# Kernel tuning notes

Hardware: AMD Instinct MI355X
Metric: run time of the kernel (lower is better)

## Reference

```python
import jax, jax.numpy as jnp
import numpy as np

B, S, F, U = 64, 512, 128, 512          # seq_length == units (required for broadcast in original code)
SIGDIM = F + F * F                       # level-2 truncated signature dimension
GRID_SIZE, SPLINE_ORDER = 5, 3           # efficient-KAN style defaults
NB = GRID_SIZE + SPLINE_ORDER            # number of b-spline basis functions per input feature
LN_EPS = 1e-3                            # keras LayerNormalization default epsilon


def _make_grid():
    h = 2.0 / GRID_SIZE  # uniform grid on [-1, 1], extended by spline order
    return -1.0 + h * jnp.arange(-SPLINE_ORDER, GRID_SIZE + SPLINE_ORDER + 1, dtype=jnp.float32)


def _b_splines(x, grid):
    # x: (N, F) -> (N, F, NB) via Cox-de Boor recursion
    x = x[..., None]
    bases = ((x >= grid[:-1]) & (x < grid[1:])).astype(x.dtype)
    for p in range(1, SPLINE_ORDER + 1):
        left = (x - grid[:-(p + 1)]) / (grid[p:-1] - grid[:-(p + 1)])
        right = (grid[p + 1:] - x) / (grid[p + 1:] - grid[1:-p])
        bases = left * bases[..., :-1] + right * bases[..., 1:]
    return bases


def _kan_linear(x, base_w, spline_w, grid):
    # KANLinear, no bias / no layernorm: silu base branch + b-spline branch
    lead = x.shape[:-1]
    base = jax.nn.silu(x) @ base_w                                  # (..., U)
    b = _b_splines(x.reshape(-1, x.shape[-1]), grid)                # (N, F, NB)
    spl = jnp.einsum('nfk,ufk->nu', b, spline_w).reshape(*lead, base_w.shape[1])
    return base + spl


def _signature2(x):
    # level-2 path signature of piecewise-linear path x: (B, S, F) -> (B, F + F*F)
    dx = x[:, 1:] - x[:, :-1]                                       # (B, S-1, F)
    s1 = dx.sum(axis=1)                                             # (B, F)
    cs = jnp.cumsum(dx, axis=1)
    prev = jnp.concatenate([jnp.zeros_like(cs[:, :1]), cs[:, :-1]], axis=1)
    s2 = jnp.einsum('bti,btj->bij', prev + 0.5 * dx, dx)            # (B, F, F)
    return jnp.concatenate([s1, s2.reshape(x.shape[0], -1)], axis=-1)


def _grkan(sig, w1, b1, w2, b2, w3, b3, w4, b4, ws, bs, gamma, beta):
    # gated residual network mapping signature -> softmax attention weights (B, U)
    h = jax.nn.elu(sig @ w1 + b1)
    h = h @ w2 + b2
    glu = jax.nn.sigmoid(h @ w3 + b3) * (h @ w4 + b4)
    y = sig @ ws + bs + glu
    mu = jnp.mean(y, axis=-1, keepdims=True)
    var = jnp.var(y, axis=-1, keepdims=True)
    y = (y - mu) / jnp.sqrt(var + LN_EPS) * gamma + beta
    return jax.nn.softmax(y, axis=-1)


def setup_inputs() -> dict:
    key = jax.random.key(0)
    ks = jax.random.split(key, 24)
    n = lambda k, shp, s=0.02: jax.random.normal(k, shp, dtype=jnp.float32) * s
    inp = {
        'inputs': jax.random.normal(ks[0], (B, S, F), dtype=jnp.float32),
        'h_prev': jax.random.normal(ks[1], (B, U), dtype=jnp.float32),
        'c_prev': jax.random.normal(ks[2], (B, U), dtype=jnp.float32),
        'time_kernel': n(ks[3], (S, 1), 0.1),
        'kan_base_w': n(ks[4], (F, U)),
        'kan_spline_w': n(ks[5], (U, F, NB)),
        'g_w1': n(ks[6], (SIGDIM, U)), 'g_b1': jnp.zeros((U,), jnp.float32),
        'g_w2': n(ks[7], (U, U)), 'g_b2': jnp.zeros((U,), jnp.float32),
        'g_w3': n(ks[8], (U, U)), 'g_b3': jnp.zeros((U,), jnp.float32),
        'g_w4': n(ks[9], (U, U)), 'g_b4': jnp.zeros((U,), jnp.float32),
        'g_skip_w': n(ks[10], (SIGDIM, U)), 'g_skip_b': jnp.zeros((U,), jnp.float32),
        'ln_gamma': jnp.ones((U,), jnp.float32), 'ln_beta': jnp.zeros((U,), jnp.float32),
        'wf': n(ks[11], (2 * U, U)), 'bf': jnp.zeros((U,), jnp.float32),
        'wi': n(ks[12], (2 * U, U)), 'bi': jnp.zeros((U,), jnp.float32),
        'wc': n(ks[13], (2 * U, U)), 'bc': jnp.zeros((U,), jnp.float32),
        'wo': n(ks[14], (2 * U, U)), 'bo': jnp.zeros((U,), jnp.float32),
    }
    return inp


def reference(inputs, h_prev, c_prev, time_kernel, kan_base_w, kan_spline_w,
              g_w1, g_b1, g_w2, g_b2, g_w3, g_b3, g_w4, g_b4, g_skip_w, g_skip_b,
              ln_gamma, ln_beta, wf, bf, wi, bi, wc, bc, wo, bo):
    grid = _make_grid()
    weighted = time_kernel * inputs                                  # (B,S,F)
    sig = _signature2(weighted)                                      # (B,SIGDIM)
    attn = _grkan(sig, g_w1, g_b1, g_w2, g_b2, g_w3, g_b3, g_w4, g_b4,
                  g_skip_w, g_skip_b, ln_gamma, ln_beta)             # (B,S) since U==S
    kan_out = _kan_linear(weighted, kan_base_w, kan_spline_w, grid)  # (B,S,U)
    attended = kan_out * attn[..., None]                             # (B,S,U)
    current = attended.mean(axis=1)                                  # (B,U)
    combined = jnp.concatenate([current, h_prev], axis=-1)           # (B,2U)
    f = jax.nn.sigmoid(combined @ wf + bf)
    i = jax.nn.sigmoid(combined @ wi + bi)
    cand = jnp.tanh(combined @ wc + bc)
    o = jax.nn.sigmoid(combined @ wo + bo)
    c_new = f * c_prev + i * cand
    h_new = o * jnp.tanh(c_new)
    return h_new, c_new
```

## Files before the change

kernel.cpp:

```cpp
#include <hip/hip_runtime.h>
#include <math.h>

#define BB 64
#define SS 512
#define FF 128
#define UU 512
#define NBB 8
#define SIGDIM (FF + FF*FF)
#define K3 16512
#define KK 1152
#define NCH 32

typedef __attribute__((ext_vector_type(8))) __bf16 bf16x8;
typedef __attribute__((ext_vector_type(4))) float f32x4;

__device__ __forceinline__ unsigned short f2bf(float x) {
    unsigned int u = __float_as_uint(x);
    unsigned int r = u + 0x7FFFu + ((u >> 16) & 1u);
    return (unsigned short)(r >> 16);
}

__device__ __forceinline__ float sigmoidf(float x) { return 1.0f / (1.0f + expf(-x)); }

__global__ void k_wprep(const float* __restrict__ splw, const float* __restrict__ basew,
                        const float* __restrict__ h_prev,
                        unsigned short* __restrict__ Wt, unsigned short* __restrict__ comb_b) {
    int idx = blockIdx.x * 256 + threadIdx.x;
    if (idx >= UU * KK) return;
    int u = idx / KK, c = idx % KK;
    float v = (c < 1024) ? splw[(size_t)u * 1024 + c] : basew[(size_t)(c - 1024) * UU + u];
    Wt[idx] = f2bf(v);
    if (idx < BB * UU) {
        int b = idx >> 9, uu = idx & 511;
        comb_b[(size_t)b * 1024 + 512 + uu] = f2bf(h_prev[idx]);
    }
}

__global__ __launch_bounds__(256) void k_wt3(const float* __restrict__ w2, const float* __restrict__ w3,
                                             const float* __restrict__ w4, const float* __restrict__ wf,
                                             const float* __restrict__ wi, const float* __restrict__ wc,
                                             const float* __restrict__ wo,
                                             unsigned short* __restrict__ W2t,
                                             unsigned short* __restrict__ W3t,
                                             unsigned short* __restrict__ W4t,
                                             unsigned short* __restrict__ Wgt) {
    int kt = blockIdx.x, ut = blockIdx.y, z = blockIdx.z;
    int Kdim = (z < 3) ? 512 : 1024;
    if (kt * 64 >= Kdim) return;
    const float* src;
    unsigned short* dst;
    switch (z) {
        case 0: src = w2; dst = W2t; break;
        case 1: src = w3; dst = W3t; break;
        case 2: src = w4; dst = W4t; break;
        case 3: src = wf; dst = Wgt; break;
        case 4: src = wi; dst = Wgt + (size_t)512 * 1024; break;
        case 5: src = wc; dst = Wgt + (size_t)1024 * 1024; break;
        default: src = wo; dst = Wgt + (size_t)1536 * 1024; break;
    }
    __shared__ float tile[64][65];
    int tid = threadIdx.x;
    int k0 = kt * 64, u0 = ut * 64;
#pragma unroll
    for (int p = 0; p < 16; ++p) {
        int e = p * 256 + tid;
        int kk = e >> 6, uu = e & 63;
        tile[kk][uu] = src[(size_t)(k0 + kk) * UU + u0 + uu];
    }
    __syncthreads();
#pragma unroll
    for (int p = 0; p < 16; ++p) {
        int e = p * 256 + tid;
        int uu = e >> 6, kk = e & 63;
        dst[(size_t)(u0 + uu) * Kdim + k0 + kk] = f2bf(tile[kk][uu]);
    }
}

__global__ __launch_bounds__(256) void k_wt2(const float* __restrict__ w1,
                                             const float* __restrict__ gsw,
                                             unsigned short* __restrict__ W1t,
                                             unsigned short* __restrict__ Wst) {
    int kt = blockIdx.x, ut = blockIdx.y, mat = blockIdx.z;
    const float* src = mat ? gsw : w1;
    unsigned short* dst = mat ? Wst : W1t;
    __shared__ float tile[64][65];
    int tid = threadIdx.x;
    int k0 = kt * 64, u0 = ut * 64;
#pragma unroll
    for (int p = 0; p < 16; ++p) {
        int e = p * 256 + tid;
        int kk = e >> 6, uu = e & 63;
        tile[kk][uu] = src[(size_t)(k0 + kk) * UU + u0 + uu];
    }
    __syncthreads();
#pragma unroll
    for (int p = 0; p < 16; ++p) {
        int e = p * 256 + tid;
        int uu = e >> 6, kk = e & 63;
        dst[(size_t)(u0 + uu) * K3 + k0 + kk] = f2bf(tile[kk][uu]);
    }
}

__global__ __launch_bounds__(256) void k_adprep(const float* __restrict__ inp,
                                                const float* __restrict__ tk,
                                                unsigned short* __restrict__ aT,
                                                unsigned short* __restrict__ dT) {
    int tt0 = blockIdx.x * 64, f0 = blockIdx.y * 64, b = blockIdx.z;
    __shared__ float aS[64][65], dS[64][65];
    __shared__ float tkS[65];
    int tid = threadIdx.x;
    if (tid < 65) { int t = tt0 + tid; tkS[tid] = (t < SS) ? tk[t] : 0.f; }
    __syncthreads();
    const float* ib = inp + (size_t)b * SS * FF;
    float tk0 = tk[0];
    for (int e = tid; e < 64 * 64; e += 256) {
        int tt = e >> 6, ff = e & 63;
        int t = tt0 + tt;
        int f = f0 + ff;
        float av = 0.f, dv = 0.f;
        if (t < SS - 1) {
            float wa = tkS[tt] * ib[(size_t)t * FF + f];
            float wn = tkS[tt + 1] * ib[(size_t)(t + 1) * FF + f];
            float w0 = tk0 * ib[f];
            av = 0.5f * (wa + wn) - w0;
            dv = wn - wa;
        }
        aS[tt][ff] = av; dS[tt][ff] = dv;
    }
    __syncthreads();
    for (int e = tid; e < 64 * 64; e += 256) {
        int ff = e >> 6, tt = e & 63;
        size_t o = ((size_t)b * FF + f0 + ff) * SS + tt0 + tt;
        aT[o] = f2bf(aS[tt][ff]);
        dT[o] = f2bf(dS[tt][ff]);
    }
}

__global__ __launch_bounds__(256) void k_sig_mfma(const unsigned short* __restrict__ aT,
                                                  const unsigned short* __restrict__ dT,
                                                  float* __restrict__ s2part) {
    int kc = blockIdx.x, b = blockIdx.y;
    int tid = threadIdx.x, lane = tid & 63;
    int wv = __builtin_amdgcn_readfirstlane(tid >> 6);
    int wrow = (wv & 1) * 64, wcol = (wv >> 1) * 64;
    int k0 = kc * 128;
    const unsigned short* pa = aT + ((size_t)b * FF + wrow + (lane & 15)) * SS + k0 + (lane >> 4) * 8;
    const unsigned short* pd = dT + ((size_t)b * FF + wcol + (lane & 15)) * SS + k0 + (lane >> 4) * 8;
    f32x4 acc[4][4];
#pragma unroll
    for (int i = 0; i < 4; ++i)
#pragma unroll
        for (int j = 0; j < 4; ++j) acc[i][j] = (f32x4)(0.f);
#pragma unroll
    for (int t = 0; t < 4; ++t) {
        bf16x8 af[4], df[4];
#pragma unroll
        for (int rt = 0; rt < 4; ++rt) af[rt] = *(const bf16x8*)(pa + (size_t)rt * 16 * SS + t * 32);
#pragma unroll
        for (int ct = 0; ct < 4; ++ct) df[ct] = *(const bf16x8*)(pd + (size_t)ct * 16 * SS + t * 32);
#pragma unroll
        for (int rt = 0; rt < 4; ++rt)
#pragma unroll
            for (int ct = 0; ct < 4; ++ct)
                acc[rt][ct] = __builtin_amdgcn_mfma_f32_16x16x32_bf16(af[rt], df[ct], acc[rt][ct], 0, 0, 0);
    }
    float* outp = s2part + ((size_t)kc * BB + b) * (FF * FF);
    int quad = lane >> 4, col = lane & 15;
#pragma unroll
    for (int rt = 0; rt < 4; ++rt)
#pragma unroll
        for (int ct = 0; ct < 4; ++ct)
#pragma unroll
            for (int reg = 0; reg < 4; ++reg)
                outp[(wrow + rt * 16 + quad * 4 + reg) * FF + wcol + ct * 16 + col] = acc[rt][ct][reg];
}

__global__ void k_sig_reduce(const float* __restrict__ inp, const float* __restrict__ tk,
                             const float* __restrict__ s2part, unsigned short* __restrict__ sigb) {
    int idx = blockIdx.x * 256 + threadIdx.x;
    if (idx >= BB * SIGDIM) return;
    int b = idx / SIGDIM, r = idx % SIGDIM;
    float v;
    if (r < FF) {
        v = tk[SS - 1] * inp[((size_t)b * SS + SS - 1) * FF + r] - tk[0] * inp[(size_t)b * SS * FF + r];
    } else {
        int ij = r - FF;
        v = 0.f;
#pragma unroll
        for (int c = 0; c < 4; ++c) v += s2part[((size_t)c * BB + b) * (FF * FF) + ij];
    }
    sigb[idx] = f2bf(v);
}

__global__ __launch_bounds__(64) void k_sig_direct(const unsigned short* __restrict__ sigb,
                                                   const unsigned short* __restrict__ W1t,
                                                   const unsigned short* __restrict__ Wst,
                                                   const float* __restrict__ b1,
                                                   unsigned short* __restrict__ h1b,
                                                   float* __restrict__ skippre) {
    int lane = threadIdx.x;
    int mt = blockIdx.x, nt = blockIdx.y, mat = blockIdx.z;
    const unsigned short* Bp = mat ? Wst : W1t;
    const unsigned short* pa = sigb + (size_t)(mt * 16 + (lane & 15)) * K3 + (lane >> 4) * 8;
    const unsigned short* pb = Bp + (size_t)(nt * 16 + (lane & 15)) * K3 + (lane >> 4) * 8;
    f32x4 acc0 = (f32x4)(0.f), acc1 = (f32x4)(0.f);
#pragma unroll 8
    for (int t = 0; t < K3 / 32; t += 2) {
        bf16x8 a0 = *(const bf16x8*)(pa + t * 32);
        bf16x8 b0 = *(const bf16x8*)(pb + t * 32);
        bf16x8 a1 = *(const bf16x8*)(pa + t * 32 + 32);
        bf16x8 b1v = *(const bf16x8*)(pb + t * 32 + 32);
        acc0 = __builtin_amdgcn_mfma_f32_16x16x32_bf16(a0, b0, acc0, 0, 0, 0);
        acc1 = __builtin_amdgcn_mfma_f32_16x16x32_bf16(a1, b1v, acc1, 0, 0, 0);
    }
    int col = lane & 15, quad = lane >> 4;
    int j = nt * 16 + col;
    if (mat == 0) {
        float bb = b1[j];
#pragma unroll
        for (int reg = 0; reg < 4; ++reg) {
            int row = mt * 16 + quad * 4 + reg;
            float v = acc0[reg] + acc1[reg] + bb;
            h1b[(size_t)row * UU + j] = f2bf(v > 0.f ? v : expf(v) - 1.0f);
        }
    } else {
#pragma unroll
        for (int reg = 0; reg < 4; ++reg) {
            int row = mt * 16 + quad * 4 + reg;
            skippre[(size_t)row * UU + j] = acc0[reg] + acc1[reg];
        }
    }
}

__global__ __launch_bounds__(64) void k_h2_direct(const unsigned short* __restrict__ h1b,
                                                  const unsigned short* __restrict__ W2t,
                                                  const float* __restrict__ b2,
                                                  unsigned short* __restrict__ h2b) {
    int lane = threadIdx.x;
    int mt = blockIdx.x, nt = blockIdx.y;
    const unsigned short* pa = h1b + (size_t)(mt * 16 + (lane & 15)) * 512 + (lane >> 4) * 8;
    const unsigned short* pb = W2t + (size_t)(nt * 16 + (lane & 15)) * 512 + (lane >> 4) * 8;
    f32x4 acc0 = (f32x4)(0.f), acc1 = (f32x4)(0.f);
#pragma unroll
    for (int t = 0; t < 16; t += 2) {
        bf16x8 a0 = *(const bf16x8*)(pa + t * 32);
        bf16x8 b0 = *(const bf16x8*)(pb + t * 32);
        bf16x8 a1 = *(const bf16x8*)(pa + t * 32 + 32);
        bf16x8 b1v = *(const bf16x8*)(pb + t * 32 + 32);
        acc0 = __builtin_amdgcn_mfma_f32_16x16x32_bf16(a0, b0, acc0, 0, 0, 0);
        acc1 = __builtin_amdgcn_mfma_f32_16x16x32_bf16(a1, b1v, acc1, 0, 0, 0);
    }
    int col = lane & 15, quad = lane >> 4;
    int j = nt * 16 + col;
    float bb = b2[j];
#pragma unroll
    for (int reg = 0; reg < 4; ++reg) {
        int row = mt * 16 + quad * 4 + reg;
        h2b[(size_t)row * UU + j] = f2bf(acc0[reg] + acc1[reg] + bb);
    }
}

__global__ __launch_bounds__(64) void k_glu_direct(const unsigned short* __restrict__ h2b,
                                                   const unsigned short* __restrict__ W3t,
                                                   const unsigned short* __restrict__ W4t,
                                                   const float* __restrict__ b3,
                                                   const float* __restrict__ b4,
                                                   const float* __restrict__ skippre,
                                                   const float* __restrict__ skb,
                                                   float* __restrict__ yv) {
    int lane = threadIdx.x;
    int mt = blockIdx.x, nt = blockIdx.y;
    const unsigned short* pa = h2b + (size_t)(mt * 16 + (lane & 15)) * 512 + (lane >> 4) * 8;
    const unsigned short* pb3 = W3t + (size_t)(nt * 16 + (lane & 15)) * 512 + (lane >> 4) * 8;
    const unsigned short* pb4 = W4t + (size_t)(nt * 16 + (lane & 15)) * 512 + (lane >> 4) * 8;
    f32x4 acc3 = (f32x4)(0.f), acc4 = (f32x4)(0.f);
#pragma unroll
    for (int t = 0; t < 16; ++t) {
        bf16x8 a = *(const bf16x8*)(pa + t * 32);
        bf16x8 b3f = *(const bf16x8*)(pb3 + t * 32);
        bf16x8 b4f = *(const bf16x8*)(pb4 + t * 32);
        acc3 = __builtin_amdgcn_mfma_f32_16x16x32_bf16(a, b3f, acc3, 0, 0, 0);
        acc4 = __builtin_amdgcn_mfma_f32_16x16x32_bf16(a, b4f, acc4, 0, 0, 0);
    }
    int col = lane & 15, quad = lane >> 4;
    int j = nt * 16 + col;
    float bb3 = b3[j], bb4 = b4[j], sb = skb[j];
#pragma unroll
    for (int reg = 0; reg < 4; ++reg) {
        int row = mt * 16 + quad * 4 + reg;
        float g = sigmoidf(acc3[reg] + bb3);
        yv[(size_t)row * UU + j] = skippre[(size_t)row * UU + j] + sb + g * (acc4[reg] + bb4);
    }
}

__device__ __forceinline__ float block_sum(float v, float* red) {
    int tid = threadIdx.x;
#pragma unroll
    for (int off = 32; off > 0; off >>= 1) v += __shfl_down(v, off);
    __syncthreads();
    if ((tid & 63) == 0) red[tid >> 6] = v;
    __syncthreads();
    float r = red[0];
#pragma unroll
    for (int i = 1; i < 8; ++i) r += red[i];
    return r;
}
__device__ __forceinline__ float block_max(float v, float* red) {
    int tid = threadIdx.x;
#pragma unroll
    for (int off = 32; off > 0; off >>= 1) v = fmaxf(v, __shfl_down(v, off));
    __syncthreads();
    if ((tid & 63) == 0) red[tid >> 6] = v;
    __syncthreads();
    float r = red[0];
#pragma unroll
    for (int i = 1; i < 8; ++i) r = fmaxf(r, red[i]);
    return r;
}

__global__ void k_lnsm(const float* __restrict__ yv, const float* __restrict__ gamma,
                       const float* __restrict__ beta, float* __restrict__ attn) {
    int b = blockIdx.x, u = threadIdx.x;
    __shared__ float red[8];
    float v = yv[(size_t)b * UU + u];
    float mu = block_sum(v, red) * (1.0f / UU);
    float d = v - mu;
    float var = block_sum(d * d, red) * (1.0f / UU);
    float z = d * rsqrtf(var + 1e-3f) * gamma[u] + beta[u];
    float m = block_max(z, red);
    float e = expf(z - m);
    float Z = block_sum(e, red);
    attn[(size_t)b * UU + u] = e / Z;
}

__global__ __launch_bounds__(128) void k_attn_red(const float* __restrict__ inp,
                                                  const float* __restrict__ tk,
                                                  const float* __restrict__ attn,
                                                  float* __restrict__ Apart) {
    int b = blockIdx.x, ch = blockIdx.y;
    int f = threadIdx.x;
    __shared__ float attnS[16], tkS[16];
    if (f < 16) { attnS[f] = attn[(size_t)b * UU + ch * 16 + f]; tkS[f] = tk[ch * 16 + f]; }
    __syncthreads();
    const float* ib = inp + ((size_t)b * SS + ch * 16) * FF + f;
    float acc[9] = {};
#pragma unroll
    for (int s = 0; s < 16; ++s) {
        float w = tkS[s] * ib[(size_t)s * FF];
        float a = attnS[s];
        float t = (w + 2.2f) * 2.5f;
        float cf = floorf(fminf(fmaxf(t, -2.f), 13.f));
        int c = (int)cf;
        float u = t - cf;
        float u2 = u * u, u3 = u2 * u;
        float p0 = u3 * (1.f / 6.f);
        float p1 = (-3.f * u3 + 3.f * u2 + 3.f * u + 1.f) * (1.f / 6.f);
        float p2 = (3.f * u3 - 6.f * u2 + 4.f) * (1.f / 6.f);
        float onemu = 1.f - u;
        float p3 = onemu * onemu * onemu * (1.f / 6.f);
#pragma unroll
        for (int k2 = 0; k2 < 8; ++k2) {
            int d = c - k2;
            float v = (d == 0) ? p0 : (d == 1) ? p1 : (d == 2) ? p2 : (d == 3) ? p3 : 0.f;
            acc[k2] += a * v;
        }
        acc[8] += a * (w * sigmoidf(w));
    }
    float* op = Apart + ((size_t)ch * BB + b) * KK;
    float4 v0 = { acc[0], acc[1], acc[2], acc[3] };
    float4 v1 = { acc[4], acc[5], acc[6], acc[7] };
    *(float4*)(op + f * 8) = v0;
    *(float4*)(op + f * 8 + 4) = v1;
    op[1024 + f] = acc[8];
}

__global__ void k_ared_red(const float* __restrict__ Apart, unsigned short* __restrict__ Aredb) {
    int idx = blockIdx.x * 256 + threadIdx.x;
    if (idx >= BB * KK) return;
    int b = idx / KK, c = idx % KK;
    float s = 0.f;
#pragma unroll
    for (int ch = 0; ch < NCH; ++ch) s += Apart[((size_t)ch * BB + b) * KK + c];
    Aredb[idx] = f2bf(s * (1.0f / SS));
}

__global__ __launch_bounds__(64) void k_cur_direct(const unsigned short* __restrict__ Aredb,
                                                   const unsigned short* __restrict__ Wt,
                                                   unsigned short* __restrict__ comb_b) {
    int lane = threadIdx.x;
    int mt = blockIdx.x, nt = blockIdx.y;
    const unsigned short* pa = Aredb + (size_t)(mt * 16 + (lane & 15)) * KK + (lane >> 4) * 8;
    const unsigned short* pb = Wt + (size_t)(nt * 16 + (lane & 15)) * KK + (lane >> 4) * 8;
    f32x4 acc0 = (f32x4)(0.f), acc1 = (f32x4)(0.f);
#pragma unroll 6
    for (int t = 0; t < KK / 32; t += 2) {
        bf16x8 a0 = *(const bf16x8*)(pa + t * 32);
        bf16x8 b0 = *(const bf16x8*)(pb + t * 32);
        bf16x8 a1 = *(const bf16x8*)(pa + t * 32 + 32);
        bf16x8 b1v = *(const bf16x8*)(pb + t * 32 + 32);
        acc0 = __builtin_amdgcn_mfma_f32_16x16x32_bf16(a0, b0, acc0, 0, 0, 0);
        acc1 = __builtin_amdgcn_mfma_f32_16x16x32_bf16(a1, b1v, acc1, 0, 0, 0);
    }
    int col = lane & 15, quad = lane >> 4;
    int j = nt * 16 + col;
#pragma unroll
    for (int reg = 0; reg < 4; ++reg) {
        int row = mt * 16 + quad * 4 + reg;
        comb_b[(size_t)row * 1024 + j] = f2bf(acc0[reg] + acc1[reg]);
    }
}

__global__ __launch_bounds__(64) void k_gates_direct(const unsigned short* __restrict__ comb_b,
                                                     const unsigned short* __restrict__ Wgt,
                                                     float* __restrict__ gates) {
    int lane = threadIdx.x;
    int mt = blockIdx.x, nt = blockIdx.y;
    const unsigned short* pa = comb_b + (size_t)(mt * 16 + (lane & 15)) * 1024 + (lane >> 4) * 8;
    const unsigned short* pb = Wgt + (size_t)(nt * 16 + (lane & 15)) * 1024 + (lane >> 4) * 8;
    f32x4 acc0 = (f32x4)(0.f), acc1 = (f32x4)(0.f);
#pragma unroll 8
    for (int t = 0; t < 32; t += 2) {
        bf16x8 a0 = *(const bf16x8*)(pa + t * 32);
        bf16x8 b0 = *(const bf16x8*)(pb + t * 32);
        bf16x8 a1 = *(const bf16x8*)(pa + t * 32 + 32);
        bf16x8 b1v = *(const bf16x8*)(pb + t * 32 + 32);
        acc0 = __builtin_amdgcn_mfma_f32_16x16x32_bf16(a0, b0, acc0, 0, 0, 0);
        acc1 = __builtin_amdgcn_mfma_f32_16x16x32_bf16(a1, b1v, acc1, 0, 0, 0);
    }
    int col = lane & 15, quad = lane >> 4;
    int j = nt * 16 + col;
#pragma unroll
    for (int reg = 0; reg < 4; ++reg) {
        int row = mt * 16 + quad * 4 + reg;
        gates[(size_t)row * 2048 + j] = acc0[reg] + acc1[reg];
    }
}

__global__ void k_cell(const float* __restrict__ gates,
                       const float* __restrict__ bf_, const float* __restrict__ bi_,
                       const float* __restrict__ bc_, const float* __restrict__ bo_,
                       const float* __restrict__ c_prev, float* __restrict__ out) {
    int idx = blockIdx.x * 256 + threadIdx.x;
    if (idx >= BB * UU) return;
    int b = idx >> 9, u = idx & 511;
    const float* g = gates + (size_t)b * 2048;
    float f = sigmoidf(g[u] + bf_[u]);
    float ii = sigmoidf(g[512 + u] + bi_[u]);
    float cd = tanhf(g[1024 + u] + bc_[u]);
    float o = sigmoidf(g[1536 + u] + bo_[u]);
    float cn = f * c_prev[idx] + ii * cd;
    out[idx] = o * tanhf(cn);
    out[(size_t)BB * UU + idx] = cn;
}

extern "C" void kernel_launch(void* const* d_in, const int* in_sizes, int n_in,
                              void* d_out, int out_size, void* d_ws, size_t ws_size,
                              hipStream_t stream) {
    const float* inp   = (const float*)d_in[0];
    const float* hprev = (const float*)d_in[1];
    const float* cprev = (const float*)d_in[2];
    const float* tk    = (const float*)d_in[3];
    const float* basew = (const float*)d_in[4];
    const float* splw  = (const float*)d_in[5];
    const float* gw1   = (const float*)d_in[6];
    const float* gb1   = (const float*)d_in[7];
    const float* gw2   = (const float*)d_in[8];
    const float* gb2   = (const float*)d_in[9];
    const float* gw3   = (const float*)d_in[10];
    const float* gb3   = (const float*)d_in[11];
    const float* gw4   = (const float*)d_in[12];
    const float* gb4   = (const float*)d_in[13];
    const float* gsw   = (const float*)d_in[14];
    const float* gsb   = (const float*)d_in[15];
    const float* lng   = (const float*)d_in[16];
    const float* lnb   = (const float*)d_in[17];
    const float* wf    = (const float*)d_in[18];
    const float* bf_   = (const float*)d_in[19];
    const float* wi    = (const float*)d_in[20];
    const float* bi_   = (const float*)d_in[21];
    const float* wc    = (const float*)d_in[22];
    const float* bc_   = (const float*)d_in[23];
    const float* wo    = (const float*)d_in[24];
    const float* bo_   = (const float*)d_in[25];
    float* out = (float*)d_out;

    float* ws = (float*)d_ws;
    size_t o = 0;
    unsigned short* W1t = (unsigned short*)(ws + o); o += (size_t)UU * K3 / 2;
    unsigned short* Wst = (unsigned short*)(ws + o); o += (size_t)UU * K3 / 2;
    unsigned short* Wt  = (unsigned short*)(ws + o); o += (size_t)UU * KK / 2;
    float* s2part   = ws + o; o += (size_t)4 * BB * FF * FF;
    unsigned short* aT = (unsigned short*)(ws + o); o += (size_t)BB * FF * SS / 2;
    unsigned short* dT = (unsigned short*)(ws + o); o += (size_t)BB * FF * SS / 2;
    unsigned short* sigb = (unsigned short*)(ws + o); o += (size_t)BB * K3 / 2;
    float* skippre  = ws + o; o += (size_t)BB * UU;
    unsigned short* h1b = (unsigned short*)(ws + o); o += (size_t)BB * UU / 2;
    unsigned short* h2b = (unsigned short*)(ws + o); o += (size_t)BB * UU / 2;
    float* yv       = ws + o; o += (size_t)BB * UU;
    float* attn     = ws + o; o += (size_t)BB * UU;
    float* Apart    = ws + o; o += (size_t)NCH * BB * KK;
    unsigned short* Aredb = (unsigned short*)(ws + o); o += (size_t)BB * KK / 2;
    unsigned short* W2t = (unsigned short*)(ws + o); o += (size_t)512 * 512 / 2;
    unsigned short* W3t = (unsigned short*)(ws + o); o += (size_t)512 * 512 / 2;
    unsigned short* W4t = (unsigned short*)(ws + o); o += (size_t)512 * 512 / 2;
    unsigned short* Wgt = (unsigned short*)(ws + o); o += (size_t)2048 * 1024 / 2;
    unsigned short* comb_b = (unsigned short*)(ws + o); o += (size_t)BB * 1024 / 2;
    float* gates    = ws + o; o += (size_t)BB * 2048;
    (void)ws_size; (void)in_sizes; (void)n_in; (void)out_size;

    k_wprep<<<(UU * KK + 255) / 256, 256, 0, stream>>>(splw, basew, hprev, Wt, comb_b);
    k_wt3<<<dim3(16, 8, 7), 256, 0, stream>>>(gw2, gw3, gw4, wf, wi, wc, wo, W2t, W3t, W4t, Wgt);
    k_wt2<<<dim3(K3 / 64, UU / 64, 2), 256, 0, stream>>>(gw1, gsw, W1t, Wst);
    k_adprep<<<dim3(8, 2, BB), 256, 0, stream>>>(inp, tk, aT, dT);
    k_sig_mfma<<<dim3(4, BB), 256, 0, stream>>>(aT, dT, s2part);
    k_sig_reduce<<<(BB * SIGDIM + 255) / 256, 256, 0, stream>>>(inp, tk, s2part, sigb);
    k_sig_direct<<<dim3(4, 32, 2), 64, 0, stream>>>(sigb, W1t, Wst, gb1, h1b, skippre);
    k_h2_direct<<<dim3(4, 32), 64, 0, stream>>>(h1b, W2t, gb2, h2b);
    k_glu_direct<<<dim3(4, 32), 64, 0, stream>>>(h2b, W3t, W4t, gb3, gb4, skippre, gsb, yv);
    k_lnsm<<<BB, UU, 0, stream>>>(yv, lng, lnb, attn);
    k_attn_red<<<dim3(BB, NCH), 128, 0, stream>>>(inp, tk, attn, Apart);
    k_ared_red<<<(BB * KK + 255) / 256, 256, 0, stream>>>(Apart, Aredb);
    k_cur_direct<<<dim3(4, 32), 64, 0, stream>>>(Aredb, Wt, comb_b);
    k_gates_direct<<<dim3(4, 128), 64, 0, stream>>>(comb_b, Wgt, gates);
    k_cell<<<(BB * UU + 255) / 256, 256, 0, stream>>>(gates, bf_, bi_, bc_, bo_, cprev, out);
}
```

Measured before the change: 300.7 us.

## Fuse attention-weighted KAN reduction into one kernel using transposed bf16 weighted inputs

k_adprep now also writes the time-weighted input transposed to (B,F,S) in bf16. A new k_kan_red kernel reads it contiguously and reduces over the full sequence with wavefront shuffles, replacing the chunked partial-sum kernel and its separate reduction pass. This removes the large Apart buffer and one launch, at the cost of an extra bf16 write in k_adprep. The weighted input is also rounded to bf16 before the spline evaluation, which lowers precision.

```diff
diff --git a/kernel.cpp b/kernel.cpp
--- a/kernel.cpp
+++ b/kernel.cpp
@@ -9,9 +9,9 @@
 #define SIGDIM (FF + FF*FF)
 #define K3 16512
 #define KK 1152
-#define NCH 32
 
 typedef __attribute__((ext_vector_type(8))) __bf16 bf16x8;
+typedef __attribute__((ext_vector_type(8))) unsigned short u16x8;
 typedef __attribute__((ext_vector_type(4))) float f32x4;
 
 __device__ __forceinline__ unsigned short f2bf(float x) {
@@ -104,9 +104,10 @@
 __global__ __launch_bounds__(256) void k_adprep(const float* __restrict__ inp,
                                                 const float* __restrict__ tk,
                                                 unsigned short* __restrict__ aT,
-                                                unsigned short* __restrict__ dT) {
+                                                unsigned short* __restrict__ dT,
+                                                unsigned short* __restrict__ wT) {
     int tt0 = blockIdx.x * 64, f0 = blockIdx.y * 64, b = blockIdx.z;
-    __shared__ float aS[64][65], dS[64][65];
+    __shared__ float aS[64][65], dS[64][65], wS[64][65];
     __shared__ float tkS[65];
     int tid = threadIdx.x;
     if (tid < 65) { int t = tt0 + tid; tkS[tid] = (t < SS) ? tk[t] : 0.f; }
@@ -117,15 +118,15 @@
         int tt = e >> 6, ff = e & 63;
         int t = tt0 + tt;
         int f = f0 + ff;
+        float wv = tkS[tt] * ib[(size_t)t * FF + f];
         float av = 0.f, dv = 0.f;
         if (t < SS - 1) {
-            float wa = tkS[tt] * ib[(size_t)t * FF + f];
             float wn = tkS[tt + 1] * ib[(size_t)(t + 1) * FF + f];
             float w0 = tk0 * ib[f];
-            av = 0.5f * (wa + wn) - w0;
-            dv = wn - wa;
+            av = 0.5f * (wv + wn) - w0;
+            dv = wn - wv;
         }
-        aS[tt][ff] = av; dS[tt][ff] = dv;
+        aS[tt][ff] = av; dS[tt][ff] = dv; wS[tt][ff] = wv;
     }
     __syncthreads();
     for (int e = tid; e < 64 * 64; e += 256) {
@@ -133,6 +134,7 @@
         size_t o = ((size_t)b * FF + f0 + ff) * SS + tt0 + tt;
         aT[o] = f2bf(aS[tt][ff]);
         dT[o] = f2bf(dS[tt][ff]);
+        wT[o] = f2bf(wS[tt][ff]);
     }
 }
 
@@ -333,21 +335,24 @@
     attn[(size_t)b * UU + u] = e / Z;
 }
 
-__global__ __launch_bounds__(128) void k_attn_red(const float* __restrict__ inp,
-                                                  const float* __restrict__ tk,
-                                                  const float* __restrict__ attn,
-                                                  float* __restrict__ Apart) {
-    int b = blockIdx.x, ch = blockIdx.y;
-    int f = threadIdx.x;
-    __shared__ float attnS[16], tkS[16];
-    if (f < 16) { attnS[f] = attn[(size_t)b * UU + ch * 16 + f]; tkS[f] = tk[ch * 16 + f]; }
-    __syncthreads();
-    const float* ib = inp + ((size_t)b * SS + ch * 16) * FF + f;
+__global__ __launch_bounds__(256) void k_kan_red(const unsigned short* __restrict__ wT,
+                                                 const float* __restrict__ attn,
+                                                 unsigned short* __restrict__ Aredb) {
+    int b = blockIdx.x;
+    int lane = threadIdx.x & 63;
+    int f = blockIdx.y * 4 + (threadIdx.x >> 6);
+
+    const u16x8 wv = *(const u16x8*)(wT + ((size_t)b * FF + f) * SS + lane * 8);
+    const float* ap = attn + (size_t)b * UU + lane * 8;
+    float4 a0 = *(const float4*)ap;
+    float4 a1 = *(const float4*)(ap + 4);
+
     float acc[9] = {};
 #pragma unroll
-    for (int s = 0; s < 16; ++s) {
-        float w = tkS[s] * ib[(size_t)s * FF];
-        float a = attnS[s];
+    for (int s = 0; s < 8; ++s) {
+        float w = __uint_as_float((unsigned int)wv[s] << 16);
+        float a = (s < 4) ? ((s == 0) ? a0.x : (s == 1) ? a0.y : (s == 2) ? a0.z : a0.w)
+                          : ((s == 4) ? a1.x : (s == 5) ? a1.y : (s == 6) ? a1.z : a1.w);
         float t = (w + 2.2f) * 2.5f;
         float cf = floorf(fminf(fmaxf(t, -2.f), 13.f));
         int c = (int)cf;
@@ -366,22 +371,21 @@
         }
         acc[8] += a * (w * sigmoidf(w));
     }
-    float* op = Apart + ((size_t)ch * BB + b) * KK;
-    float4 v0 = { acc[0], acc[1], acc[2], acc[3] };
-    float4 v1 = { acc[4], acc[5], acc[6], acc[7] };
-    *(float4*)(op + f * 8) = v0;
-    *(float4*)(op + f * 8 + 4) = v1;
-    op[1024 + f] = acc[8];
-}
-
-__global__ void k_ared_red(const float* __restrict__ Apart, unsigned short* __restrict__ Aredb) {
-    int idx = blockIdx.x * 256 + threadIdx.x;
-    if (idx >= BB * KK) return;
-    int b = idx / KK, c = idx % KK;
-    float s = 0.f;
-#pragma unroll
-    for (int ch = 0; ch < NCH; ++ch) s += Apart[((size_t)ch * BB + b) * KK + c];
-    Aredb[idx] = f2bf(s * (1.0f / SS));
+
+#pragma unroll
+    for (int off = 1; off < 64; off <<= 1) {
+#pragma unroll
+        for (int k = 0; k < 9; ++k) acc[k] += __shfl_xor(acc[k], off);
+    }
+
+    if (lane == 0) {
+        const float sc = 1.0f / SS;
+        u16x8 ov;
+#pragma unroll
+        for (int k = 0; k < 8; ++k) ov[k] = f2bf(acc[k] * sc);
+        *(u16x8*)(Aredb + (size_t)b * KK + f * 8) = ov;
+        Aredb[(size_t)b * KK + 1024 + f] = f2bf(acc[8] * sc);
+    }
 }
 
 __global__ __launch_bounds__(64) void k_cur_direct(const unsigned short* __restrict__ Aredb,
@@ -492,13 +496,13 @@
     float* s2part   = ws + o; o += (size_t)4 * BB * FF * FF;
     unsigned short* aT = (unsigned short*)(ws + o); o += (size_t)BB * FF * SS / 2;
     unsigned short* dT = (unsigned short*)(ws + o); o += (size_t)BB * FF * SS / 2;
+    unsigned short* wT = (unsigned short*)(ws + o); o += (size_t)BB * FF * SS / 2;
     unsigned short* sigb = (unsigned short*)(ws + o); o += (size_t)BB * K3 / 2;
     float* skippre  = ws + o; o += (size_t)BB * UU;
     unsigned short* h1b = (unsigned short*)(ws + o); o += (size_t)BB * UU / 2;
     unsigned short* h2b = (unsigned short*)(ws + o); o += (size_t)BB * UU / 2;
     float* yv       = ws + o; o += (size_t)BB * UU;
     float* attn     = ws + o; o += (size_t)BB * UU;
-    float* Apart    = ws + o; o += (size_t)NCH * BB * KK;
     unsigned short* Aredb = (unsigned short*)(ws + o); o += (size_t)BB * KK / 2;
     unsigned short* W2t = (unsigned short*)(ws + o); o += (size_t)512 * 512 / 2;
     unsigned short* W3t = (unsigned short*)(ws + o); o += (size_t)512 * 512 / 2;
@@ -511,15 +515,14 @@
     k_wprep<<<(UU * KK + 255) / 256, 256, 0, stream>>>(splw, basew, hprev, Wt, comb_b);
     k_wt3<<<dim3(16, 8, 7), 256, 0, stream>>>(gw2, gw3, gw4, wf, wi, wc, wo, W2t, W3t, W4t, Wgt);
     k_wt2<<<dim3(K3 / 64, UU / 64, 2), 256, 0, stream>>>(gw1, gsw, W1t, Wst);
-    k_adprep<<<dim3(8, 2, BB), 256, 0, stream>>>(inp, tk, aT, dT);
+    k_adprep<<<dim3(8, 2, BB), 256, 0, stream>>>(inp, tk, aT, dT, wT);
     k_sig_mfma<<<dim3(4, BB), 256, 0, stream>>>(aT, dT, s2part);
     k_sig_reduce<<<(BB * SIGDIM + 255) / 256, 256, 0, stream>>>(inp, tk, s2part, sigb);
     k_sig_direct<<<dim3(4, 32, 2), 64, 0, stream>>>(sigb, W1t, Wst, gb1, h1b, skippre);
     k_h2_direct<<<dim3(4, 32), 64, 0, stream>>>(h1b, W2t, gb2, h2b);
     k_glu_direct<<<dim3(4, 32), 64, 0, stream>>>(h2b, W3t, W4t, gb3, gb4, skippre, gsb, yv);
     k_lnsm<<<BB, UU, 0, stream>>>(yv, lng, lnb, attn);
-    k_attn_red<<<dim3(BB, NCH), 128, 0, stream>>>(inp, tk, attn, Apart);
-    k_ared_red<<<(BB * KK + 255) / 256, 256, 0, stream>>>(Apart, Aredb);
+    k_kan_red<<<dim3(BB, FF / 4), 256, 0, stream>>>(wT, attn, Aredb);
     k_cur_direct<<<dim3(4, 32), 64, 0, stream>>>(Aredb, Wt, comb_b);
     k_gates_direct<<<dim3(4, 128), 64, 0, stream>>>(comb_b, Wgt, gates);
     k_cell<<<(BB * UU + 255) / 256, 256, 0, stream>>>(gates, bf_, bi_, bc_, bo_, cprev, out);
```

Result: no change. 302.2 us (+0.5%).
